# Optimization experiments

Hardware: AMD Instinct MI355X
Metric: run time of the kernel (lower is better)

The kernel has to match this reference:

```python
import jax, jax.numpy as jnp
import numpy as np

EMBED_DIM = 512
NUM_HEADS = 8
HEAD_DIM = EMBED_DIM // NUM_HEADS
SCALE = HEAD_DIM ** -0.5
B, N = 4, 2048


def setup_inputs() -> dict:
    key = jax.random.key(0)
    ks = jax.random.split(key, 6)
    x = jax.random.normal(ks[0], (B, N, EMBED_DIM), dtype=jnp.float32)
    mask = jnp.ones((B, N, N), dtype=jnp.int32)
    # nn.Linear params: weight [out, in], bias [out]
    lim_qkv = 1.0 / np.sqrt(EMBED_DIM)
    qkv_w = jax.random.uniform(ks[1], (3 * EMBED_DIM, EMBED_DIM), jnp.float32, -lim_qkv, lim_qkv)
    qkv_b = jax.random.uniform(ks[2], (3 * EMBED_DIM,), jnp.float32, -lim_qkv, lim_qkv)
    proj_w = jax.random.uniform(ks[3], (EMBED_DIM, EMBED_DIM), jnp.float32, -lim_qkv, lim_qkv)
    proj_b = jax.random.uniform(ks[4], (EMBED_DIM,), jnp.float32, -lim_qkv, lim_qkv)
    return {"x": x, "qkv_w": qkv_w, "qkv_b": qkv_b, "proj_w": proj_w, "proj_b": proj_b, "mask": mask}


def reference(x, qkv_w, qkv_b, proj_w, proj_b, mask):
    Bb, Nn, C = x.shape
    qkv = (jnp.einsum('bnc,oc->bno', x, qkv_w) + qkv_b).reshape(Bb, Nn, 3, NUM_HEADS, HEAD_DIM)
    qkv = jnp.transpose(qkv, (2, 0, 3, 1, 4))
    q, k, v = qkv[0], qkv[1], qkv[2]
    # full score matrix [B,H,N,N] (faithful to the unfused original)
    attn = jnp.einsum('bhnd,bhmd->bhnm', q, k) * SCALE
    attn = jnp.where(mask[:, None, :, :] == 0, -jnp.inf, attn)
    attn = jax.nn.softmax(attn, axis=-1)
    out = jnp.einsum('bhnm,bhmd->bhnd', attn, v)
    out = jnp.transpose(out, (0, 2, 1, 3)).reshape(Bb, Nn, C)
    out = jnp.einsum('bnc,oc->bno', out, proj_w) + proj_b
    return out
```

## Files before the change

kernel.cpp:

```cpp
#include <hip/hip_runtime.h>
#include <hip/hip_bf16.h>
#include <stdint.h>

#define NB 4
#define NH 8
#define SEQ 2048
#define HD 64
#define CDIM 512

using bf16 = __hip_bfloat16;
typedef __attribute__((ext_vector_type(8))) short short8;
typedef __attribute__((ext_vector_type(4))) short short4_t;
typedef __attribute__((ext_vector_type(4))) float f32x4;

#define NEG_BIG (-3.0e38f)
#define SOFT_C 0.18033688011112042f

__device__ __forceinline__ short bf16_bits(float x) {
  return __builtin_bit_cast(short, __float2bfloat16(x));
}

__device__ __forceinline__ void gld_lds16(const void* g, void* l) {
  __builtin_amdgcn_global_load_lds(
      (const __attribute__((address_space(1))) unsigned int*)g,
      (__attribute__((address_space(3))) unsigned int*)l, 16, 0, 0);
}

#define X4 1048576
#define Q4 196608
#define P4 65536
__global__ __launch_bounds__(256) void prep_cvt(const float* __restrict__ x,
                                                const float* __restrict__ wq,
                                                const float* __restrict__ wp,
                                                short* __restrict__ xb,
                                                short* __restrict__ wqb,
                                                short* __restrict__ wpb) {
  int idx = blockIdx.x * 256 + threadIdx.x;
  int stride = gridDim.x * 256;
  for (int i = idx; i < X4 + Q4 + P4; i += stride) {
    const float* src; short* dst; int off;
    if (i < X4)            { src = x;  dst = xb;  off = i; }
    else if (i < X4 + Q4)  { src = wq; dst = wqb; off = i - X4; }
    else                   { src = wp; dst = wpb; off = i - X4 - Q4; }
    f32x4 v = *(const f32x4*)(src + (size_t)off * 4);
    short4_t o;
    o[0] = bf16_bits(v[0]); o[1] = bf16_bits(v[1]);
    o[2] = bf16_bits(v[2]); o[3] = bf16_bits(v[3]);
    *(short4_t*)(dst + (size_t)off * 4) = o;
  }
}

__global__ __launch_bounds__(256) void qkv_union(const short* __restrict__ Xb,
                                                 const short* __restrict__ Wb,
                                                 const float* __restrict__ bias,
                                                 const int* __restrict__ mask,
                                                 unsigned long long* __restrict__ bits,
                                                 bf16* __restrict__ q,
                                                 bf16* __restrict__ k,
                                                 bf16* __restrict__ vt) {
  __shared__ short Alds[128][40];
  __shared__ short Blds[128][40];
  const int tid = threadIdx.x;
  const int lane = tid & 63;
  const int w = tid >> 6;

  if (blockIdx.x < 512) {
    int wave_g = blockIdx.x * 4 + w;
#pragma unroll 1
    for (int i = 0; i < 32; i++) {
      size_t c = (size_t)i * 2048 + wave_g;
      size_t base = c * 256;
      int v0 = mask[base + 0 * 64 + lane];
      int v1 = mask[base + 1 * 64 + lane];
      int v2 = mask[base + 2 * 64 + lane];
      int v3 = mask[base + 3 * 64 + lane];
      unsigned long long w0 = __ballot(v0 != 0);
      unsigned long long w1 = __ballot(v1 != 0);
      unsigned long long w2 = __ballot(v2 != 0);
      unsigned long long w3 = __ballot(v3 != 0);
      if (lane == 0) {
        bits[c * 4 + 0] = w0; bits[c * 4 + 1] = w1;
        bits[c * 4 + 2] = w2; bits[c * 4 + 3] = w3;
      }
    }
    return;
  }

  const int g = blockIdx.x - 512;
  const int wm = w >> 1, wn = w & 1;
  const int row0 = (g & 63) * 128;
  const int col0 = (g >> 6) * 128;
  const bool isv = (col0 >= 1024);

  f32x4 acc[4][4] = {};
  const int lr = tid >> 2;
  const int lc = (tid & 3) * 8;
  const int cl = lane & 15;
  const int quad = lane >> 4;
  const int koff = quad * 8;

  for (int kk = 0; kk < 512; kk += 32) {
    *(short8*)&Alds[lr][lc]      = *(const short8*)&Xb[(size_t)(row0 + lr) * 512 + kk + lc];
    *(short8*)&Alds[lr + 64][lc] = *(const short8*)&Xb[(size_t)(row0 + lr + 64) * 512 + kk + lc];
    *(short8*)&Blds[lr][lc]      = *(const short8*)&Wb[(size_t)(col0 + lr) * 512 + kk + lc];
    *(short8*)&Blds[lr + 64][lc] = *(const short8*)&Wb[(size_t)(col0 + lr + 64) * 512 + kk + lc];
    __syncthreads();
    short8 a[4], b[4];
#pragma unroll
    for (int i = 0; i < 4; i++) a[i] = *(const short8*)&Alds[wm * 64 + i * 16 + cl][koff];
#pragma unroll
    for (int j = 0; j < 4; j++) b[j] = *(const short8*)&Blds[wn * 64 + j * 16 + cl][koff];
    if (!isv) {
#pragma unroll
      for (int i = 0; i < 4; i++)
#pragma unroll
        for (int j = 0; j < 4; j++)
          acc[i][j] = __builtin_amdgcn_mfma_f32_16x16x32_bf16(a[i], b[j], acc[i][j], 0, 0, 0);
    } else {
#pragma unroll
      for (int i = 0; i < 4; i++)
#pragma unroll
        for (int j = 0; j < 4; j++)
          acc[i][j] = __builtin_amdgcn_mfma_f32_16x16x32_bf16(b[j], a[i], acc[i][j], 0, 0, 0);
    }
    __syncthreads();
  }

  if (!isv) {
#pragma unroll
    for (int i = 0; i < 4; i++) {
#pragma unroll
      for (int j = 0; j < 4; j++) {
        int col = col0 + wn * 64 + j * 16 + cl;
        float bv = bias[col];
        int which = col >> 9;
        int c = col & 511;
        int h = c >> 6, d = c & 63;
#pragma unroll
        for (int r = 0; r < 4; r++) {
          int row = row0 + wm * 64 + i * 16 + quad * 4 + r;
          int bb = row >> 11, n = row & 2047;
          float val = acc[i][j][r] + bv;
          size_t bh = (size_t)bb * NH + h;
          if (which == 0)      q[(bh * SEQ + n) * HD + d] = __float2bfloat16(val * SOFT_C);
          else                 k[(bh * SEQ + n) * HD + d] = __float2bfloat16(val);
        }
      }
    }
  } else {
#pragma unroll
    for (int i = 0; i < 4; i++) {
#pragma unroll
      for (int j = 0; j < 4; j++) {
        int nrow = row0 + wm * 64 + i * 16 + cl;
        int bb = nrow >> 11, n = nrow & 2047;
#pragma unroll
        for (int r = 0; r < 4; r++) {
          int col = col0 + wn * 64 + j * 16 + quad * 4 + r;
          float bv = bias[col];
          int c = col & 511;
          int h = c >> 6, d = c & 63;
          float val = acc[i][j][r] + bv;
          size_t bh = (size_t)bb * NH + h;
          vt[(bh * HD + d) * SEQ + n] = __float2bfloat16(val);
        }
      }
    }
  }
}

__global__ __launch_bounds__(256) void flash_attn(const bf16* __restrict__ qg,
                                                  const bf16* __restrict__ kg,
                                                  const bf16* __restrict__ vg,
                                                  const unsigned long long* __restrict__ mbits,
                                                  bf16* __restrict__ attn_out) {
  __shared__ short Klds[64][64];
  __shared__ short Vlds[64][64];
  __shared__ short Plds[4][16][72];
  __shared__ unsigned long long Mlds[64];

  const int tid = threadIdx.x;
  const int lane = tid & 63;
  const int w = tid >> 6;
  const int qt = blockIdx.x;
  const int h = blockIdx.y;
  const int b = blockIdx.z;

  const size_t bh = (size_t)b * NH + h;
  const bf16* qp = qg + bh * SEQ * HD;
  const bf16* kp = kg + bh * SEQ * HD;
  const bf16* vp = vg + bh * HD * SEQ;

  const int cl = lane & 15;
  const int quad = lane >> 4;
  const int koff = quad * 8;
  const int qrow_w = qt * 64 + w * 16;

  const int c0 = ((quad ^ (cl & 7)) * 8);

  const int st_row = lane >> 3;
  const int st_chunk = (lane & 7) ^ st_row;
  const int st_col = st_chunk * 8;

  short8 aq0 = *(const short8*)&qp[(size_t)(qrow_w + cl) * HD + koff];
  short8 aq1 = *(const short8*)&qp[(size_t)(qrow_w + cl) * HD + 32 + koff];

  f32x4 o[4] = {};
  float l_l = 0.f;

  for (int kt = 0; kt < 32; kt++) {
    const int kb = kt * 64;
#pragma unroll
    for (int t = 0; t < 2; t++) {
      int rbase = w * 16 + t * 8;
      gld_lds16(&kp[(size_t)(kb + rbase + st_row) * HD + st_col], &Klds[rbase][0]);
      gld_lds16(&vp[(size_t)(rbase + st_row) * SEQ + kb + st_col], &Vlds[rbase][0]);
    }
    if (tid < 64) Mlds[tid] = mbits[((size_t)b * SEQ + qt * 64 + tid) * (SEQ / 64) + kt];
    __syncthreads();

    f32x4 s[4];
#pragma unroll
    for (int nb = 0; nb < 4; nb++) {
      short8 k0 = *(const short8*)&Klds[nb * 16 + cl][c0];
      short8 k1 = *(const short8*)&Klds[nb * 16 + cl][c0 ^ 32];
      f32x4 z = {0.f, 0.f, 0.f, 0.f};
      z = __builtin_amdgcn_mfma_f32_16x16x32_bf16(k0, aq0, z, 0, 0, 0);
      s[nb] = __builtin_amdgcn_mfma_f32_16x16x32_bf16(k1, aq1, z, 0, 0, 0);
    }

    unsigned long long wd = Mlds[w * 16 + cl];
    if (wd != ~0ULL) {
#pragma unroll
      for (int nb = 0; nb < 4; nb++)
#pragma unroll
        for (int r = 0; r < 4; r++)
          if (!((wd >> (nb * 16 + quad * 4 + r)) & 1ULL)) s[nb][r] = NEG_BIG;
    }

    float ps = 0.f;
#pragma unroll
    for (int nb = 0; nb < 4; nb++)
#pragma unroll
      for (int r = 0; r < 4; r++) {
        float p = __builtin_amdgcn_exp2f(s[nb][r]);
        s[nb][r] = p;
        ps += p;
      }
    ps += __shfl_xor(ps, 16);
    ps += __shfl_xor(ps, 32);
    l_l += ps;

#pragma unroll
    for (int nb = 0; nb < 4; nb++) {
      short4_t pk;
      pk[0] = bf16_bits(s[nb][0]); pk[1] = bf16_bits(s[nb][1]);
      pk[2] = bf16_bits(s[nb][2]); pk[3] = bf16_bits(s[nb][3]);
      *(short4_t*)&Plds[w][cl][nb * 16 + quad * 4] = pk;
    }

#pragma unroll
    for (int ks = 0; ks < 2; ks++) {
      short8 pa = *(const short8*)&Plds[w][cl][ks * 32 + koff];
      const int vc = c0 ^ (ks * 32);
#pragma unroll
      for (int db = 0; db < 4; db++) {
        short8 vb = *(const short8*)&Vlds[db * 16 + cl][vc];
        o[db] = __builtin_amdgcn_mfma_f32_16x16x32_bf16(pa, vb, o[db], 0, 0, 0);
      }
    }
    __syncthreads();
  }

  float inv = 1.0f / l_l;
#pragma unroll
  for (int r = 0; r < 4; r++) {
    float ir = __shfl(inv, (lane & 48) + quad * 4 + r);
    int row = qrow_w + quad * 4 + r;
#pragma unroll
    for (int db = 0; db < 4; db++) {
      float val = o[db][r] * ir;
      attn_out[((size_t)b * SEQ + row) * CDIM + h * 64 + db * 16 + cl] = __float2bfloat16(val);
    }
  }
}

__global__ __launch_bounds__(256) void proj_gemm(const bf16* __restrict__ X,
                                                 const short* __restrict__ Wb,
                                                 const float* __restrict__ bias,
                                                 float* __restrict__ out) {
  __shared__ short Alds[128][40];
  __shared__ short Blds[128][40];
  const int tid = threadIdx.x;
  const int lane = tid & 63;
  const int w = tid >> 6;
  const int wm = w >> 1, wn = w & 1;
  const int row0 = blockIdx.x * 128;
  const int col0 = blockIdx.y * 128;

  f32x4 acc[4][4] = {};
  const int lr = tid >> 2;
  const int lc = (tid & 3) * 8;
  const int cl = lane & 15;
  const int koff = (lane >> 4) * 8;

  for (int kk = 0; kk < 512; kk += 32) {
    *(short8*)&Alds[lr][lc]      = *(const short8*)&X[(size_t)(row0 + lr) * 512 + kk + lc];
    *(short8*)&Alds[lr + 64][lc] = *(const short8*)&X[(size_t)(row0 + lr + 64) * 512 + kk + lc];
    *(short8*)&Blds[lr][lc]      = *(const short8*)&Wb[(size_t)(col0 + lr) * 512 + kk + lc];
    *(short8*)&Blds[lr + 64][lc] = *(const short8*)&Wb[(size_t)(col0 + lr + 64) * 512 + kk + lc];
    __syncthreads();
    short8 a[4], b[4];
#pragma unroll
    for (int i = 0; i < 4; i++) a[i] = *(const short8*)&Alds[wm * 64 + i * 16 + cl][koff];
#pragma unroll
    for (int j = 0; j < 4; j++) b[j] = *(const short8*)&Blds[wn * 64 + j * 16 + cl][koff];
#pragma unroll
    for (int i = 0; i < 4; i++)
#pragma unroll
      for (int j = 0; j < 4; j++)
        acc[i][j] = __builtin_amdgcn_mfma_f32_16x16x32_bf16(a[i], b[j], acc[i][j], 0, 0, 0);
    __syncthreads();
  }

#pragma unroll
  for (int i = 0; i < 4; i++) {
#pragma unroll
    for (int j = 0; j < 4; j++) {
      int col = col0 + wn * 64 + j * 16 + cl;
      float bv = bias[col];
#pragma unroll
      for (int r = 0; r < 4; r++) {
        int row = row0 + wm * 64 + i * 16 + (lane >> 4) * 4 + r;
        out[(size_t)row * 512 + col] = acc[i][j][r] + bv;
      }
    }
  }
}

extern "C" void kernel_launch(void* const* d_in, const int* in_sizes, int n_in,
                              void* d_out, int out_size, void* d_ws, size_t ws_size,
                              hipStream_t stream) {
  const float* x      = (const float*)d_in[0];
  const float* qkv_w  = (const float*)d_in[1];
  const float* qkv_b  = (const float*)d_in[2];
  const float* proj_w = (const float*)d_in[3];
  const float* proj_b = (const float*)d_in[4];
  const int*   mask   = (const int*)d_in[5];
  float* out = (float*)d_out;

  char* ws = (char*)d_ws;
  bf16* q    = (bf16*)(ws);
  bf16* k    = (bf16*)(ws + 8388608);
  bf16* vt   = (bf16*)(ws + 16777216);
  bf16* attn = (bf16*)(ws + 25165824);
  short* xb  = (short*)(ws + 25165824);
  unsigned long long* mbits = (unsigned long long*)(ws + 33554432);
  short* wqb = (short*)(ws + 35651584);
  short* wpb = (short*)(ws + 37224448);

  prep_cvt<<<dim3(1280), 256, 0, stream>>>(x, qkv_w, proj_w, xb, wqb, wpb);
  qkv_union<<<dim3(512 + 768), 256, 0, stream>>>(xb, wqb, qkv_b, mask, mbits, q, k, vt);
  flash_attn<<<dim3(SEQ / 64, NH, NB), 256, 0, stream>>>(q, k, vt, mbits, attn);
  proj_gemm<<<dim3(64, 4), 256, 0, stream>>>(attn, wpb, proj_b, out);
}
```

Baseline: 229.3 us.

## Use direct global-to-LDS loads with XOR-swizzled tiles in QKV and projection GEMMs

Replaces the register-staged global-to-shared tile copies in the QKV and projection GEMMs with global_load_lds transfers into unpadded 32-wide LDS tiles. It applies an XOR swizzle on both the store column and the fragment read column to avoid bank conflicts without padding. It also restructures the softmax exp/sum into vector accumulation. This aims to cut VGPR traffic and copy instructions. The risk is that the swizzle mapping must match the direct-to-LDS lane layout exactly.

Result: no change. 226.6 us (-1.2%).

```diff
diff --git a/kernel.cpp b/kernel.cpp
--- a/kernel.cpp
+++ b/kernel.cpp
@@ -50,6 +50,7 @@
   }
 }
 
+
 __global__ __launch_bounds__(256) void qkv_union(const short* __restrict__ Xb,
                                                  const short* __restrict__ Wb,
                                                  const float* __restrict__ bias,
@@ -58,8 +59,8 @@
                                                  bf16* __restrict__ q,
                                                  bf16* __restrict__ k,
                                                  bf16* __restrict__ vt) {
-  __shared__ short Alds[128][40];
-  __shared__ short Blds[128][40];
+  __shared__ short Alds[128][32];
+  __shared__ short Blds[128][32];
   const int tid = threadIdx.x;
   const int lane = tid & 63;
   const int w = tid >> 6;
@@ -93,23 +94,27 @@
   const bool isv = (col0 >= 1024);
 
   f32x4 acc[4][4] = {};
-  const int lr = tid >> 2;
-  const int lc = (tid & 3) * 8;
   const int cl = lane & 15;
   const int quad = lane >> 4;
-  const int koff = quad * 8;
+
+  const int st_r = lane >> 2;
+  const int st_gc = (lane & 3) ^ (st_r & 3);
+  const int st_col = st_gc * 8;
+  const int fc = (quad ^ (cl & 3)) * 8;
 
   for (int kk = 0; kk < 512; kk += 32) {
-    *(short8*)&Alds[lr][lc]      = *(const short8*)&Xb[(size_t)(row0 + lr) * 512 + kk + lc];
-    *(short8*)&Alds[lr + 64][lc] = *(const short8*)&Xb[(size_t)(row0 + lr + 64) * 512 + kk + lc];
-    *(short8*)&Blds[lr][lc]      = *(const short8*)&Wb[(size_t)(col0 + lr) * 512 + kk + lc];
-    *(short8*)&Blds[lr + 64][lc] = *(const short8*)&Wb[(size_t)(col0 + lr + 64) * 512 + kk + lc];
+#pragma unroll
+    for (int t = 0; t < 2; t++) {
+      int R = w * 32 + t * 16;
+      gld_lds16(&Xb[(size_t)(row0 + R + st_r) * 512 + kk + st_col], &Alds[R][0]);
+      gld_lds16(&Wb[(size_t)(col0 + R + st_r) * 512 + kk + st_col], &Blds[R][0]);
+    }
     __syncthreads();
     short8 a[4], b[4];
 #pragma unroll
-    for (int i = 0; i < 4; i++) a[i] = *(const short8*)&Alds[wm * 64 + i * 16 + cl][koff];
-#pragma unroll
-    for (int j = 0; j < 4; j++) b[j] = *(const short8*)&Blds[wn * 64 + j * 16 + cl][koff];
+    for (int i = 0; i < 4; i++) a[i] = *(const short8*)&Alds[wm * 64 + i * 16 + cl][fc];
+#pragma unroll
+    for (int j = 0; j < 4; j++) b[j] = *(const short8*)&Blds[wn * 64 + j * 16 + cl][fc];
     if (!isv) {
 #pragma unroll
       for (int i = 0; i < 4; i++)
@@ -238,15 +243,14 @@
           if (!((wd >> (nb * 16 + quad * 4 + r)) & 1ULL)) s[nb][r] = NEG_BIG;
     }
 
-    float ps = 0.f;
-#pragma unroll
-    for (int nb = 0; nb < 4; nb++)
-#pragma unroll
-      for (int r = 0; r < 4; r++) {
-        float p = __builtin_amdgcn_exp2f(s[nb][r]);
-        s[nb][r] = p;
-        ps += p;
-      }
+    f32x4 ps4 = {0.f, 0.f, 0.f, 0.f};
+#pragma unroll
+    for (int nb = 0; nb < 4; nb++) {
+#pragma unroll
+      for (int r = 0; r < 4; r++) s[nb][r] = __builtin_amdgcn_exp2f(s[nb][r]);
+      ps4 += s[nb];
+    }
+    float ps = (ps4[0] + ps4[1]) + (ps4[2] + ps4[3]);
     ps += __shfl_xor(ps, 16);
     ps += __shfl_xor(ps, 32);
     l_l += ps;
@@ -289,8 +293,8 @@
                                                  const short* __restrict__ Wb,
                                                  const float* __restrict__ bias,
                                                  float* __restrict__ out) {
-  __shared__ short Alds[128][40];
-  __shared__ short Blds[128][40];
+  __shared__ short Alds[128][32];
+  __shared__ short Blds[128][32];
   const int tid = threadIdx.x;
   const int lane = tid & 63;
   const int w = tid >> 6;
@@ -299,22 +303,27 @@
   const int col0 = blockIdx.y * 128;
 
   f32x4 acc[4][4] = {};
-  const int lr = tid >> 2;
-  const int lc = (tid & 3) * 8;
   const int cl = lane & 15;
-  const int koff = (lane >> 4) * 8;
+  const int quad = lane >> 4;
+
+  const int st_r = lane >> 2;
+  const int st_gc = (lane & 3) ^ (st_r & 3);
+  const int st_col = st_gc * 8;
+  const int fc = (quad ^ (cl & 3)) * 8;
 
   for (int kk = 0; kk < 512; kk += 32) {
-    *(short8*)&Alds[lr][lc]      = *(const short8*)&X[(size_t)(row0 + lr) * 512 + kk + lc];
-    *(short8*)&Alds[lr + 64][lc] = *(const short8*)&X[(size_t)(row0 + lr + 64) * 512 + kk + lc];
-    *(short8*)&Blds[lr][lc]      = *(const short8*)&Wb[(size_t)(col0 + lr) * 512 + kk + lc];
-    *(short8*)&Blds[lr + 64][lc] = *(const short8*)&Wb[(size_t)(col0 + lr + 64) * 512 + kk + lc];
+#pragma unroll
+    for (int t = 0; t < 2; t++) {
+      int R = w * 32 + t * 16;
+      gld_lds16(&X[(size_t)(row0 + R + st_r) * 512 + kk + st_col], &Alds[R][0]);
+      gld_lds16(&Wb[(size_t)(col0 + R + st_r) * 512 + kk + st_col], &Blds[R][0]);
+    }
     __syncthreads();
     short8 a[4], b[4];
 #pragma unroll
-    for (int i = 0; i < 4; i++) a[i] = *(const short8*)&Alds[wm * 64 + i * 16 + cl][koff];
-#pragma unroll
-    for (int j = 0; j < 4; j++) b[j] = *(const short8*)&Blds[wn * 64 + j * 16 + cl][koff];
+    for (int i = 0; i < 4; i++) a[i] = *(const short8*)&Alds[wm * 64 + i * 16 + cl][fc];
+#pragma unroll
+    for (int j = 0; j < 4; j++) b[j] = *(const short8*)&Blds[wn * 64 + j * 16 + cl][fc];
 #pragma unroll
     for (int i = 0; i < 4; i++)
 #pragma unroll
@@ -331,7 +340,7 @@
       float bv = bias[col];
 #pragma unroll
       for (int r = 0; r < 4; r++) {
-        int row = row0 + wm * 64 + i * 16 + (lane >> 4) * 4 + r;
+        int row = row0 + wm * 64 + i * 16 + quad * 4 + r;
         out[(size_t)row * 512 + col] = acc[i][j][r] + bv;
       }
     }
```
